# Optimization experiments

Hardware: AMD Instinct MI355X
Metric: run time of the kernel (lower is better)

Reference implementation:

```python
import jax, jax.numpy as jnp
import numpy as np

B, C, H, W = 4, 32, 544, 960


def setup_inputs() -> dict:
    key = jax.random.key(0)
    k1, k2, k3 = jax.random.split(key, 3)
    tenInput = jax.random.normal(k1, (B, C, H, W), dtype=jnp.float32)
    # flows of a few pixels magnitude, typical for adjacent video frames
    tenFlow = jax.random.normal(k2, (B, 2, H, W), dtype=jnp.float32) * 4.0
    tenMetric = jax.random.normal(k3, (B, 1, H, W), dtype=jnp.float32)
    return {"tenInput": tenInput, "tenFlow": tenFlow, "tenMetric": tenMetric}


def _splat_one(x, flow):
    # x: [C', H, W] values to splat; flow: [2, H, W] (dx, dy)
    Cp, h, w = x.shape
    gy, gx = jnp.meshgrid(jnp.arange(h, dtype=flow.dtype),
                          jnp.arange(w, dtype=flow.dtype), indexing='ij')
    ox = gx + flow[0]  # fractional target x
    oy = gy + flow[1]  # fractional target y
    x0 = jnp.floor(ox)
    y0 = jnp.floor(oy)
    x1 = x0 + 1.0
    y1 = y0 + 1.0
    # bilinear corner weights (NW, NE, SW, SE), identical to CUDA kernel
    w_nw = (x1 - ox) * (y1 - oy)
    w_ne = (ox - x0) * (y1 - oy)
    w_sw = (x1 - ox) * (oy - y0)
    w_se = (ox - x0) * (oy - y0)
    xf = x.reshape(Cp, h * w)
    out = jnp.zeros((Cp, h * w), dtype=x.dtype)
    for cx, cy, wt in ((x0, y0, w_nw), (x1, y0, w_ne), (x0, y1, w_sw), (x1, y1, w_se)):
        ix = cx.astype(jnp.int32)
        iy = cy.astype(jnp.int32)
        valid = (ix >= 0) & (ix < w) & (iy >= 0) & (iy < h)
        wt = jnp.where(valid, wt, 0.0).reshape(h * w)
        idx = (jnp.clip(iy, 0, h - 1) * w + jnp.clip(ix, 0, w - 1)).reshape(h * w)
        out = out.at[:, idx].add(xf * wt[None, :])
    return out.reshape(Cp, h, w)


def softsplat(tenInput, tenFlow, tenMetric, strType):
    if strType == 'average':
        x = jnp.concatenate([tenInput, jnp.ones_like(tenInput[:, :1])], axis=1)
    elif strType == 'linear':
        x = jnp.concatenate([tenInput * tenMetric, tenMetric], axis=1)
    elif strType == 'softmax':
        m = jnp.exp(tenMetric)
        x = jnp.concatenate([tenInput * m, m], axis=1)
    else:  # 'summation'
        x = tenInput
    out = jax.vmap(_splat_one)(x, tenFlow)
    if strType != 'summation':
        norm = out[:, -1:]
        norm = jnp.where(norm == 0.0, 1.0, norm)  # tenNormalize[tenNormalize==0]=1
        out = out[:, :-1] / norm
    return out


def reference(tenInput, tenFlow, tenMetric):
    return softsplat(tenInput, tenFlow, tenMetric, 'softmax')
```

## Files before the change

### kernel.cpp

```cpp
#include <hip/hip_runtime.h>
#include <hip/hip_fp16.h>

constexpr int B = 4, C = 32, H = 544, W = 960;
constexpr int HW = H * W;
constexpr int NPIX = B * HW;

constexpr int TX = 64, TY = 32;
constexpr int PAD = 16;
constexpr int WSX = TX + 2 * PAD;
constexpr int WSY = TY + 2 * PAD;
constexpr int WPIX = WSX * WSY;
constexpr int TILES_X = W / TX;
constexpr int TILES_Y = H / TY;
constexpr int NTILES = TILES_X * TILES_Y;
constexpr int TILE = TX * TY;
constexpr int TPB = 1024;
constexpr int NW = TPB / 64;
constexpr int PPT = TILE / TPB;
constexpr int WIT = WPIX / TPB;
constexpr int CAPE = 11264;
constexpr int MAXFAR = 64;
constexpr unsigned FARCAP = 32768;

struct FarEntry { unsigned key; float a; int p; };

__global__ __launch_bounds__(256)
void far_scan(const float* __restrict__ flow,
              const float* __restrict__ metric,
              unsigned* __restrict__ counter,
              FarEntry* __restrict__ fl)
{
    int idx = blockIdx.x * blockDim.x + threadIdx.x;
    if (idx >= NPIX) return;
    int b = idx / HW;
    int p = idx - b * HW;
    int y = p / W;
    int x = p - y * W;

    float fx = flow[(size_t)(b * 2 + 0) * HW + p];
    float fy = flow[(size_t)(b * 2 + 1) * HW + p];
    if (fabsf(fx) <= 14.0f && fabsf(fy) <= 14.0f) return;

    float ox = (float)x + fx, oy = (float)y + fy;
    float x0f = floorf(ox), y0f = floorf(oy);
    int x0 = (int)x0f, y0 = (int)y0f;
    float wxh = ox - x0f, wxl = 1.0f - wxh;
    float wyh = oy - y0f, wyl = 1.0f - wyh;
    const int   cxs[4] = { x0, x0 + 1, x0,     x0 + 1 };
    const int   cys[4] = { y0, y0,     y0 + 1, y0 + 1 };
    const float wts[4] = { wxl * wyl, wxh * wyl, wxl * wyh, wxh * wyh };
    float m = __expf(metric[(size_t)b * HW + p]);

#pragma unroll
    for (int k = 0; k < 4; ++k) {
        int cx = cxs[k], cy = cys[k];
        if ((unsigned)cx >= (unsigned)W || (unsigned)cy >= (unsigned)H) continue;
        int tx0 = (cx >> 6) << 6;
        int ty0 = (cy >> 5) << 5;
        bool catchable = (x >= tx0 - PAD) && (x < tx0 + TX + PAD) &&
                         (y >= ty0 - PAD) && (y < ty0 + TY + PAD);
        if (!catchable) {
            unsigned slot = atomicAdd(counter, 1u);
            if (slot < FARCAP) {
                int tile = (cy >> 5) * TILES_X + (cx >> 6);
                unsigned lidx = (unsigned)(((cy - ty0) << 6) | (cx - tx0));
                fl[slot] = { ((unsigned)(b * NTILES + tile) << 11) | lidx,
                             wts[k] * m, p };
            }
        }
    }
}

__global__ __launch_bounds__(TPB)
void splat_csr(const float* __restrict__ inp,
               const float* __restrict__ flow,
               const float* __restrict__ metric,
               const unsigned* __restrict__ counter,
               const FarEntry* __restrict__ fl,
               float* __restrict__ out)
{
    __shared__ unsigned entries[CAPE];
    __shared__ unsigned pool[WPIX + MAXFAR];
    __shared__ int farPix[MAXFAR];
    __shared__ unsigned wsum[NW];
    __shared__ unsigned farCnt;

    unsigned* offs = pool;
    __half2*  win  = reinterpret_cast<__half2*>(pool);

    const int t    = threadIdx.x;
    const int tile = blockIdx.x;
    const int b    = blockIdx.y;
    const int tx0  = (tile % TILES_X) * TX;
    const int ty0  = (tile / TILES_X) * TY;
    const unsigned btid = (unsigned)(b * NTILES + tile);

    const float* fxp = flow + (size_t)(b * 2 + 0) * HW;
    const float* fyp = flow + (size_t)(b * 2 + 1) * HW;
    const float* mp  = metric + (size_t)b * HW;

    for (int i = t; i < TILE; i += TPB) offs[i] = 0;
    if (t == 0) farCnt = 0;
    __syncthreads();

#pragma unroll
    for (int j = 0; j < WIT; ++j) {
        int i = t + j * TPB;
        int wx = i % WSX, wy = i / WSX;
        int gx = tx0 - PAD + wx, gy = ty0 - PAD + wy;
        if ((unsigned)gx >= (unsigned)W || (unsigned)gy >= (unsigned)H) continue;
        int p = gy * W + gx;
        float ox = (float)gx + fxp[p];
        float oy = (float)gy + fyp[p];
        int lx0 = (int)floorf(ox) - tx0, ly0 = (int)floorf(oy) - ty0;
        if (lx0 < -1 || lx0 >= TX || ly0 < -1 || ly0 >= TY) continue;
#pragma unroll
        for (int k = 0; k < 4; ++k) {
            int lx = lx0 + (k & 1), ly = ly0 + (k >> 1);
            if ((unsigned)lx < (unsigned)TX && (unsigned)ly < (unsigned)TY)
                atomicAdd(&offs[(ly << 6) + lx], 1u);
        }
    }
    unsigned farN = *counter;
    if (farN > FARCAP) farN = FARCAP;
    for (unsigned e = t; e < farN; e += TPB) {
        unsigned k = fl[e].key;
        if ((k >> 11) == btid) atomicAdd(&offs[k & 2047u], 1u);
    }
    __syncthreads();

    {
        unsigned c0 = offs[2 * t], c1 = offs[2 * t + 1];
        unsigned s = c0 + c1;
        unsigned lane = t & 63, wv = t >> 6;
        unsigned incl = s;
#pragma unroll
        for (int d = 1; d < 64; d <<= 1) {
            unsigned u = __shfl_up(incl, d);
            if (lane >= (unsigned)d) incl += u;
        }
        if (lane == 63) wsum[wv] = incl;
        __syncthreads();
        if (t < 64) {
            unsigned v = (lane < NW) ? wsum[lane] : 0u;
            unsigned inc2 = v;
#pragma unroll
            for (int d = 1; d < 16; d <<= 1) {
                unsigned u = __shfl_up(inc2, d);
                if (lane >= (unsigned)d) inc2 += u;
            }
            if (lane < NW) wsum[lane] = inc2 - v;
        }
        __syncthreads();
        unsigned base = wsum[wv] + (incl - s);
        offs[2 * t]     = base;
        offs[2 * t + 1] = base + c0;
    }
    __syncthreads();

#pragma unroll
    for (int j = 0; j < WIT; ++j) {
        int i = t + j * TPB;
        int wx = i % WSX, wy = i / WSX;
        int gx = tx0 - PAD + wx, gy = ty0 - PAD + wy;
        if ((unsigned)gx >= (unsigned)W || (unsigned)gy >= (unsigned)H) continue;
        int p = gy * W + gx;
        float ox = (float)gx + fxp[p];
        float oy = (float)gy + fyp[p];
        float x0f = floorf(ox), y0f = floorf(oy);
        int lx0 = (int)x0f - tx0, ly0 = (int)y0f - ty0;
        if (lx0 < -1 || lx0 >= TX || ly0 < -1 || ly0 >= TY) continue;
        float wxh = ox - x0f, wxl = 1.0f - wxh;
        float wyh = oy - y0f, wyl = 1.0f - wyh;
        float m = __expf(mp[p]);
        const float w4[4] = { wxl * wyl, wxh * wyl, wxl * wyh, wxh * wyh };
#pragma unroll
        for (int k = 0; k < 4; ++k) {
            int lx = lx0 + (k & 1), ly = ly0 + (k >> 1);
            if ((unsigned)lx < (unsigned)TX && (unsigned)ly < (unsigned)TY) {
                unsigned pos = atomicAdd(&offs[(ly << 6) + lx], 1u);
                if (pos < CAPE) {
                    unsigned short ha = __half_as_ushort(__float2half(w4[k] * m));
                    entries[pos] = ((unsigned)i << 16) | (unsigned)ha;
                }
            }
        }
    }
    for (unsigned e = t; e < farN; e += TPB) {
        unsigned k = fl[e].key;
        if ((k >> 11) == btid) {
            unsigned pos = atomicAdd(&offs[k & 2047u], 1u);
            if (pos < CAPE) {
                unsigned idx = atomicAdd(&farCnt, 1u);
                if (idx < MAXFAR) {
                    farPix[idx] = fl[e].p;
                    unsigned short ha = __half_as_ushort(__float2half(fl[e].a));
                    entries[pos] = ((unsigned)(WPIX + idx) << 16) | (unsigned)ha;
                } else {
                    entries[pos] = 0u;
                }
            }
        }
    }
    __syncthreads();

    int qout[PPT];
    unsigned es[PPT], ee[PPT];
    float rn[PPT];
#pragma unroll
    for (int k = 0; k < PPT; ++k) {
        int sp = t + k * TPB;
        qout[k] = (ty0 + (sp >> 6)) * W + tx0 + (sp & 63);
        unsigned end = min(offs[sp], (unsigned)CAPE);
        unsigned start = min(sp ? offs[sp - 1] : 0u, (unsigned)CAPE);
        if (start > end) start = end;
        es[k] = start; ee[k] = end;
        float n = 0.0f;
        for (unsigned e = start; e < end; ++e)
            n += __half2float(__ushort_as_half((unsigned short)(entries[e] & 0xFFFFu)));
        rn[k] = (n == 0.0f) ? 1.0f : 1.0f / n;
    }

    int wp[WIT];
#pragma unroll
    for (int j = 0; j < WIT; ++j) {
        int i = t + j * TPB;
        int wx = i % WSX, wy = i / WSX;
        int gx = tx0 - PAD + wx, gy = ty0 - PAD + wy;
        wp[j] = ((unsigned)gx < (unsigned)W && (unsigned)gy < (unsigned)H)
                ? gy * W + gx : -1;
    }

    float2 pre[WIT];
    {
        const float* t0 = inp + (size_t)(b * C) * HW;
        const float* t1 = t0 + HW;
#pragma unroll
        for (int j = 0; j < WIT; ++j)
            pre[j] = (wp[j] >= 0) ? make_float2(t0[wp[j]], t1[wp[j]])
                                  : make_float2(0.f, 0.f);
    }
    unsigned nFar = farCnt;
    if (nFar > MAXFAR) nFar = MAXFAR;
    __syncthreads();

    for (int cp = 0; cp < C / 2; ++cp) {
        const float* s0 = inp + (size_t)(b * C + 2 * cp) * HW;
        const float* s1 = s0 + HW;

#pragma unroll
        for (int j = 0; j < WIT; ++j)
            win[t + j * TPB] = __floats2half2_rn(pre[j].x, pre[j].y);
        if (t < nFar) {
            int p = farPix[t];
            win[WPIX + t] = __floats2half2_rn(s0[p], s1[p]);
        }
        __syncthreads();

        if (cp + 1 < C / 2) {
            const float* t0 = inp + (size_t)(b * C + 2 * (cp + 1)) * HW;
            const float* t1 = t0 + HW;
#pragma unroll
            for (int j = 0; j < WIT; ++j)
                pre[j] = (wp[j] >= 0) ? make_float2(t0[wp[j]], t1[wp[j]])
                                      : make_float2(0.f, 0.f);
        }

        float* o0 = out + (size_t)(b * C + 2 * cp) * HW;
        float* o1 = o0 + HW;
#pragma unroll
        for (int k = 0; k < PPT; ++k) {
            __half2 acc = __floats2half2_rn(0.f, 0.f);
            for (unsigned e = es[k]; e < ee[k]; ++e) {
                unsigned ent = entries[e];
                __half2 hv = win[ent >> 16];
                __half  w  = __ushort_as_half((unsigned short)(ent & 0xFFFFu));
                acc = __hfma2(__half2half2(w), hv, acc);
            }
            int q = qout[k];
            o0[q] = __low2float(acc)  * rn[k];
            o1[q] = __high2float(acc) * rn[k];
        }
        __syncthreads();
    }
}


__global__ __launch_bounds__(256)
void splat_f32(const float* __restrict__ inp,
               const float* __restrict__ flow,
               const float* __restrict__ metric,
               float* __restrict__ out,
               float* __restrict__ norm)
{
    int idx = blockIdx.x * blockDim.x + threadIdx.x;
    if (idx >= NPIX) return;
    int b = idx / HW;
    int p = idx - b * HW;
    int y = p / W;
    int x = p - y * W;

    float fx = flow[(b * 2 + 0) * HW + p];
    float fy = flow[(b * 2 + 1) * HW + p];
    float m  = __expf(metric[b * HW + p]);

    float ox = (float)x + fx, oy = (float)y + fy;
    float x0f = floorf(ox), y0f = floorf(oy);
    int x0 = (int)x0f, y0 = (int)y0f;
    float wx1 = ox - x0f, wx0 = 1.0f - wx1;
    float wy1 = oy - y0f, wy0 = 1.0f - wy1;

    float vm[C];
    const float* inb = inp + (size_t)b * C * HW + p;
#pragma unroll
    for (int c = 0; c < C; ++c) vm[c] = inb[(size_t)c * HW] * m;

    float* outb = out + (size_t)b * C * HW;
    float* nrmb = norm + (size_t)b * HW;

    const int   cxs[4] = { x0, x0 + 1, x0,     x0 + 1 };
    const int   cys[4] = { y0, y0,     y0 + 1, y0 + 1 };
    const float wts[4] = { wx0 * wy0, wx1 * wy0, wx0 * wy1, wx1 * wy1 };

#pragma unroll
    for (int k = 0; k < 4; ++k) {
        int cx = cxs[k], cy = cys[k];
        if (cx < 0 || cx >= W || cy < 0 || cy >= H) continue;
        float wt = wts[k];
        int q = cy * W + cx;
        atomicAdd(&nrmb[q], m * wt);
#pragma unroll
        for (int c = 0; c < C; ++c)
            atomicAdd(&outb[(size_t)c * HW + q], vm[c] * wt);
    }
}

__global__ __launch_bounds__(256)
void normalize_f32(float* __restrict__ out, const float* __restrict__ norm)
{
    int t = blockIdx.x * blockDim.x + threadIdx.x;
    long long base = (long long)t * 4;
    if (base >= (long long)B * C * HW) return;
    long long b = base / ((long long)C * HW);
    long long q = base % HW;

    float4 o = *reinterpret_cast<float4*>(out + base);
    float4 n = *reinterpret_cast<const float4*>(norm + b * HW + q);
    o.x /= (n.x == 0.0f ? 1.0f : n.x);
    o.y /= (n.y == 0.0f ? 1.0f : n.y);
    o.z /= (n.z == 0.0f ? 1.0f : n.z);
    o.w /= (n.w == 0.0f ? 1.0f : n.w);
    *reinterpret_cast<float4*>(out + base) = o;
}

extern "C" void kernel_launch(void* const* d_in, const int* in_sizes, int n_in,
                              void* d_out, int out_size, void* d_ws, size_t ws_size,
                              hipStream_t stream) {
    const float* tenInput  = (const float*)d_in[0];
    const float* tenFlow   = (const float*)d_in[1];
    const float* tenMetric = (const float*)d_in[2];
    float* out = (float*)d_out;

    const size_t need = 16 + (size_t)FARCAP * sizeof(FarEntry);

    if (ws_size >= need) {
        unsigned* counter = (unsigned*)d_ws;
        FarEntry* fl = (FarEntry*)((char*)d_ws + 16);

        hipMemsetAsync(counter, 0, 16, stream);
        far_scan<<<(NPIX + 255) / 256, 256, 0, stream>>>(tenFlow, tenMetric, counter, fl);

        dim3 grid(NTILES, B);
        splat_csr<<<grid, TPB, 0, stream>>>(tenInput, tenFlow, tenMetric,
                                            counter, fl, out);
    } else {
        float* norm = (float*)d_ws;
        hipMemsetAsync(out, 0, (size_t)B * C * HW * sizeof(float), stream);
        hipMemsetAsync(norm, 0, (size_t)NPIX * sizeof(float), stream);

        int threads = 256;
        int blocks = (NPIX + threads - 1) / threads;
        splat_f32<<<blocks, threads, 0, stream>>>(tenInput, tenFlow, tenMetric, out, norm);

        long long total = (long long)B * C * HW / 4;
        normalize_f32<<<(int)((total + threads - 1) / threads), threads, 0, stream>>>(out, norm);
    }
}
```

Baseline: 205.4 us.

## Process four channels per pass and shrink halo padding to cut passes

The gather loop now handles four fp16 channels per pass instead of two, packing them into a uint2 shared-memory window. This halves the number of passes, barriers and CSR entry walks per tile. The halo pad drops from 16 to 12, which shrinks the window and the entry capacity so shared memory fits the doubled window. The far-scan threshold follows the new pad, so more pixels take the slower far-list path, and WIT becomes a ceiling division with bounds checks.

```diff
diff --git a/kernel.cpp b/kernel.cpp
--- a/kernel.cpp
+++ b/kernel.cpp
@@ -6,7 +6,7 @@
 constexpr int NPIX = B * HW;
 
 constexpr int TX = 64, TY = 32;
-constexpr int PAD = 16;
+constexpr int PAD = 12;
 constexpr int WSX = TX + 2 * PAD;
 constexpr int WSY = TY + 2 * PAD;
 constexpr int WPIX = WSX * WSY;
@@ -17,9 +17,11 @@
 constexpr int TPB = 1024;
 constexpr int NW = TPB / 64;
 constexpr int PPT = TILE / TPB;
-constexpr int WIT = WPIX / TPB;
-constexpr int CAPE = 11264;
+constexpr int WIT = (WPIX + TPB - 1) / TPB;
+constexpr int CAPE = 9728;
 constexpr int MAXFAR = 64;
+constexpr int NCH = 4;
+constexpr int NPASS = C / NCH;
 constexpr unsigned FARCAP = 32768;
 
 struct FarEntry { unsigned key; float a; int p; };
@@ -39,7 +41,7 @@
 
     float fx = flow[(size_t)(b * 2 + 0) * HW + p];
     float fy = flow[(size_t)(b * 2 + 1) * HW + p];
-    if (fabsf(fx) <= 14.0f && fabsf(fy) <= 14.0f) return;
+    if (fabsf(fx) <= (float)(PAD - 2) && fabsf(fy) <= (float)(PAD - 2)) return;
 
     float ox = (float)x + fx, oy = (float)y + fy;
     float x0f = floorf(ox), y0f = floorf(oy);
@@ -80,13 +82,13 @@
                float* __restrict__ out)
 {
     __shared__ unsigned entries[CAPE];
-    __shared__ unsigned pool[WPIX + MAXFAR];
+    __shared__ __align__(16) unsigned pool[2 * (WPIX + MAXFAR)];
     __shared__ int farPix[MAXFAR];
     __shared__ unsigned wsum[NW];
     __shared__ unsigned farCnt;
 
     unsigned* offs = pool;
-    __half2*  win  = reinterpret_cast<__half2*>(pool);
+    uint2*    win2 = reinterpret_cast<uint2*>(pool);
 
     const int t    = threadIdx.x;
     const int tile = blockIdx.x;
@@ -106,6 +108,7 @@
 #pragma unroll
     for (int j = 0; j < WIT; ++j) {
         int i = t + j * TPB;
+        if (i >= WPIX) break;
         int wx = i % WSX, wy = i / WSX;
         int gx = tx0 - PAD + wx, gy = ty0 - PAD + wy;
         if ((unsigned)gx >= (unsigned)W || (unsigned)gy >= (unsigned)H) continue;
@@ -161,6 +164,7 @@
 #pragma unroll
     for (int j = 0; j < WIT; ++j) {
         int i = t + j * TPB;
+        if (i >= WPIX) break;
         int wx = i % WSX, wy = i / WSX;
         int gx = tx0 - PAD + wx, gy = ty0 - PAD + wy;
         if ((unsigned)gx >= (unsigned)W || (unsigned)gy >= (unsigned)H) continue;
@@ -225,61 +229,78 @@
 #pragma unroll
     for (int j = 0; j < WIT; ++j) {
         int i = t + j * TPB;
-        int wx = i % WSX, wy = i / WSX;
-        int gx = tx0 - PAD + wx, gy = ty0 - PAD + wy;
-        wp[j] = ((unsigned)gx < (unsigned)W && (unsigned)gy < (unsigned)H)
-                ? gy * W + gx : -1;
-    }
-
-    float2 pre[WIT];
+        wp[j] = -1;
+        if (i < WPIX) {
+            int wx = i % WSX, wy = i / WSX;
+            int gx = tx0 - PAD + wx, gy = ty0 - PAD + wy;
+            if ((unsigned)gx < (unsigned)W && (unsigned)gy < (unsigned)H)
+                wp[j] = gy * W + gx;
+        }
+    }
+
+    float4 pre[WIT];
     {
-        const float* t0 = inp + (size_t)(b * C) * HW;
-        const float* t1 = t0 + HW;
+        const float* s0 = inp + (size_t)(b * C) * HW;
 #pragma unroll
         for (int j = 0; j < WIT; ++j)
-            pre[j] = (wp[j] >= 0) ? make_float2(t0[wp[j]], t1[wp[j]])
-                                  : make_float2(0.f, 0.f);
+            pre[j] = (wp[j] >= 0)
+                   ? make_float4(s0[wp[j]], s0[HW + wp[j]],
+                                 s0[2 * HW + wp[j]], s0[3 * HW + wp[j]])
+                   : make_float4(0.f, 0.f, 0.f, 0.f);
     }
     unsigned nFar = farCnt;
     if (nFar > MAXFAR) nFar = MAXFAR;
     __syncthreads();
 
-    for (int cp = 0; cp < C / 2; ++cp) {
-        const float* s0 = inp + (size_t)(b * C + 2 * cp) * HW;
-        const float* s1 = s0 + HW;
-
-#pragma unroll
-        for (int j = 0; j < WIT; ++j)
-            win[t + j * TPB] = __floats2half2_rn(pre[j].x, pre[j].y);
+    for (int cp = 0; cp < NPASS; ++cp) {
+        const float* s0 = inp + (size_t)(b * C + NCH * cp) * HW;
+
+#pragma unroll
+        for (int j = 0; j < WIT; ++j) {
+            int i = t + j * TPB;
+            if (i < WPIX) {
+                __half2 h01 = __floats2half2_rn(pre[j].x, pre[j].y);
+                __half2 h23 = __floats2half2_rn(pre[j].z, pre[j].w);
+                win2[i] = make_uint2(*reinterpret_cast<unsigned*>(&h01),
+                                     *reinterpret_cast<unsigned*>(&h23));
+            }
+        }
         if (t < nFar) {
             int p = farPix[t];
-            win[WPIX + t] = __floats2half2_rn(s0[p], s1[p]);
+            __half2 h01 = __floats2half2_rn(s0[p], s0[HW + p]);
+            __half2 h23 = __floats2half2_rn(s0[2 * HW + p], s0[3 * HW + p]);
+            win2[WPIX + t] = make_uint2(*reinterpret_cast<unsigned*>(&h01),
+                                        *reinterpret_cast<unsigned*>(&h23));
         }
         __syncthreads();
 
-        if (cp + 1 < C / 2) {
-            const float* t0 = inp + (size_t)(b * C + 2 * (cp + 1)) * HW;
-            const float* t1 = t0 + HW;
+        if (cp + 1 < NPASS) {
+            const float* n0 = inp + (size_t)(b * C + NCH * (cp + 1)) * HW;
 #pragma unroll
             for (int j = 0; j < WIT; ++j)
-                pre[j] = (wp[j] >= 0) ? make_float2(t0[wp[j]], t1[wp[j]])
-                                      : make_float2(0.f, 0.f);
-        }
-
-        float* o0 = out + (size_t)(b * C + 2 * cp) * HW;
-        float* o1 = o0 + HW;
+                pre[j] = (wp[j] >= 0)
+                       ? make_float4(n0[wp[j]], n0[HW + wp[j]],
+                                     n0[2 * HW + wp[j]], n0[3 * HW + wp[j]])
+                       : make_float4(0.f, 0.f, 0.f, 0.f);
+        }
+
+        float* o0 = out + (size_t)(b * C + NCH * cp) * HW;
 #pragma unroll
         for (int k = 0; k < PPT; ++k) {
-            __half2 acc = __floats2half2_rn(0.f, 0.f);
+            __half2 a01 = __floats2half2_rn(0.f, 0.f);
+            __half2 a23 = __floats2half2_rn(0.f, 0.f);
             for (unsigned e = es[k]; e < ee[k]; ++e) {
                 unsigned ent = entries[e];
-                __half2 hv = win[ent >> 16];
-                __half  w  = __ushort_as_half((unsigned short)(ent & 0xFFFFu));
-                acc = __hfma2(__half2half2(w), hv, acc);
+                uint2 wv = win2[ent >> 16];
+                __half2 w2 = __half2half2(__ushort_as_half((unsigned short)(ent & 0xFFFFu)));
+                a01 = __hfma2(w2, *reinterpret_cast<__half2*>(&wv.x), a01);
+                a23 = __hfma2(w2, *reinterpret_cast<__half2*>(&wv.y), a23);
             }
             int q = qout[k];
-            o0[q] = __low2float(acc)  * rn[k];
-            o1[q] = __high2float(acc) * rn[k];
+            o0[q]          = __low2float(a01)  * rn[k];
+            o0[HW + q]     = __high2float(a01) * rn[k];
+            o0[2 * HW + q] = __low2float(a23)  * rn[k];
+            o0[3 * HW + q] = __high2float(a23) * rn[k];
         }
         __syncthreads();
     }
```

Result: faster. 198.4 us (-3.4%).

## Gather source values directly from global memory instead of staging half2 windows in LDS

Applied to the files above, without the earlier changes.

Drops the per-channel-pair shared-memory window of half2 source values and its barriers. Each output pixel now walks its CSR entry list and gathers fp32 inputs straight from global memory for 8 channels at a time, accumulating in fp32. Corner weights are now cached in registers during the counting pass so the fill pass does not recompute flow, and the padding shrinks from 16 to 12, which reduces both the window and the entry capacity. The trade is that LDS reuse of the window is replaced by repeated global or cache gathers. It also relies on the far-scan path to catch the larger set of long-range flows that the smaller padding no longer covers.

```diff
diff --git a/kernel.cpp b/kernel.cpp
--- a/kernel.cpp
+++ b/kernel.cpp
@@ -6,7 +6,7 @@
 constexpr int NPIX = B * HW;
 
 constexpr int TX = 64, TY = 32;
-constexpr int PAD = 16;
+constexpr int PAD = 12;
 constexpr int WSX = TX + 2 * PAD;
 constexpr int WSY = TY + 2 * PAD;
 constexpr int WPIX = WSX * WSY;
@@ -17,9 +17,11 @@
 constexpr int TPB = 1024;
 constexpr int NW = TPB / 64;
 constexpr int PPT = TILE / TPB;
-constexpr int WIT = WPIX / TPB;
-constexpr int CAPE = 11264;
+constexpr int WIT = (WPIX + TPB - 1) / TPB;
+constexpr int CAPE = 9728;
 constexpr int MAXFAR = 64;
+constexpr int NCH = 8;
+constexpr int NPASS = C / NCH;
 constexpr unsigned FARCAP = 32768;
 
 struct FarEntry { unsigned key; float a; int p; };
@@ -39,7 +41,7 @@
 
     float fx = flow[(size_t)(b * 2 + 0) * HW + p];
     float fy = flow[(size_t)(b * 2 + 1) * HW + p];
-    if (fabsf(fx) <= 14.0f && fabsf(fy) <= 14.0f) return;
+    if (fabsf(fx) <= (float)(PAD - 2) && fabsf(fy) <= (float)(PAD - 2)) return;
 
     float ox = (float)x + fx, oy = (float)y + fy;
     float x0f = floorf(ox), y0f = floorf(oy);
@@ -80,19 +82,17 @@
                float* __restrict__ out)
 {
     __shared__ unsigned entries[CAPE];
-    __shared__ unsigned pool[WPIX + MAXFAR];
+    __shared__ unsigned offs[TILE];
     __shared__ int farPix[MAXFAR];
     __shared__ unsigned wsum[NW];
     __shared__ unsigned farCnt;
-
-    unsigned* offs = pool;
-    __half2*  win  = reinterpret_cast<__half2*>(pool);
 
     const int t    = threadIdx.x;
     const int tile = blockIdx.x;
     const int b    = blockIdx.y;
     const int tx0  = (tile % TILES_X) * TX;
     const int ty0  = (tile / TILES_X) * TY;
+    const int rowBase = (ty0 - PAD) * W + (tx0 - PAD);
     const unsigned btid = (unsigned)(b * NTILES + tile);
 
     const float* fxp = flow + (size_t)(b * 2 + 0) * HW;
@@ -103,64 +103,13 @@
     if (t == 0) farCnt = 0;
     __syncthreads();
 
+    unsigned cr[WIT][4];
 #pragma unroll
     for (int j = 0; j < WIT; ++j) {
+#pragma unroll
+        for (int k = 0; k < 4; ++k) cr[j][k] = 0xFFFF0000u;
         int i = t + j * TPB;
-        int wx = i % WSX, wy = i / WSX;
-        int gx = tx0 - PAD + wx, gy = ty0 - PAD + wy;
-        if ((unsigned)gx >= (unsigned)W || (unsigned)gy >= (unsigned)H) continue;
-        int p = gy * W + gx;
-        float ox = (float)gx + fxp[p];
-        float oy = (float)gy + fyp[p];
-        int lx0 = (int)floorf(ox) - tx0, ly0 = (int)floorf(oy) - ty0;
-        if (lx0 < -1 || lx0 >= TX || ly0 < -1 || ly0 >= TY) continue;
-#pragma unroll
-        for (int k = 0; k < 4; ++k) {
-            int lx = lx0 + (k & 1), ly = ly0 + (k >> 1);
-            if ((unsigned)lx < (unsigned)TX && (unsigned)ly < (unsigned)TY)
-                atomicAdd(&offs[(ly << 6) + lx], 1u);
-        }
-    }
-    unsigned farN = *counter;
-    if (farN > FARCAP) farN = FARCAP;
-    for (unsigned e = t; e < farN; e += TPB) {
-        unsigned k = fl[e].key;
-        if ((k >> 11) == btid) atomicAdd(&offs[k & 2047u], 1u);
-    }
-    __syncthreads();
-
-    {
-        unsigned c0 = offs[2 * t], c1 = offs[2 * t + 1];
-        unsigned s = c0 + c1;
-        unsigned lane = t & 63, wv = t >> 6;
-        unsigned incl = s;
-#pragma unroll
-        for (int d = 1; d < 64; d <<= 1) {
-            unsigned u = __shfl_up(incl, d);
-            if (lane >= (unsigned)d) incl += u;
-        }
-        if (lane == 63) wsum[wv] = incl;
-        __syncthreads();
-        if (t < 64) {
-            unsigned v = (lane < NW) ? wsum[lane] : 0u;
-            unsigned inc2 = v;
-#pragma unroll
-            for (int d = 1; d < 16; d <<= 1) {
-                unsigned u = __shfl_up(inc2, d);
-                if (lane >= (unsigned)d) inc2 += u;
-            }
-            if (lane < NW) wsum[lane] = inc2 - v;
-        }
-        __syncthreads();
-        unsigned base = wsum[wv] + (incl - s);
-        offs[2 * t]     = base;
-        offs[2 * t + 1] = base + c0;
-    }
-    __syncthreads();
-
-#pragma unroll
-    for (int j = 0; j < WIT; ++j) {
-        int i = t + j * TPB;
+        if (i >= WPIX) continue;
         int wx = i % WSX, wy = i / WSX;
         int gx = tx0 - PAD + wx, gy = ty0 - PAD + wy;
         if ((unsigned)gx >= (unsigned)W || (unsigned)gy >= (unsigned)H) continue;
@@ -178,11 +127,63 @@
         for (int k = 0; k < 4; ++k) {
             int lx = lx0 + (k & 1), ly = ly0 + (k >> 1);
             if ((unsigned)lx < (unsigned)TX && (unsigned)ly < (unsigned)TY) {
-                unsigned pos = atomicAdd(&offs[(ly << 6) + lx], 1u);
-                if (pos < CAPE) {
-                    unsigned short ha = __half_as_ushort(__float2half(w4[k] * m));
-                    entries[pos] = ((unsigned)i << 16) | (unsigned)ha;
-                }
+                unsigned lidx = (unsigned)((ly << 6) + lx);
+                unsigned short ha = __half_as_ushort(__float2half(w4[k] * m));
+                cr[j][k] = (lidx << 16) | (unsigned)ha;
+                atomicAdd(&offs[lidx], 1u);
+            }
+        }
+    }
+    unsigned farN = *counter;
+    if (farN > FARCAP) farN = FARCAP;
+    for (unsigned e = t; e < farN; e += TPB) {
+        unsigned k = fl[e].key;
+        if ((k >> 11) == btid) atomicAdd(&offs[k & 2047u], 1u);
+    }
+    __syncthreads();
+
+    {
+        unsigned c0 = offs[2 * t], c1 = offs[2 * t + 1];
+        unsigned s = c0 + c1;
+        unsigned lane = t & 63, wv = t >> 6;
+        unsigned incl = s;
+#pragma unroll
+        for (int d = 1; d < 64; d <<= 1) {
+            unsigned u = __shfl_up(incl, d);
+            if (lane >= (unsigned)d) incl += u;
+        }
+        if (lane == 63) wsum[wv] = incl;
+        __syncthreads();
+        if (t < 64) {
+            unsigned v = (lane < NW) ? wsum[lane] : 0u;
+            unsigned inc2 = v;
+#pragma unroll
+            for (int d = 1; d < 16; d <<= 1) {
+                unsigned u = __shfl_up(inc2, d);
+                if (lane >= (unsigned)d) inc2 += u;
+            }
+            if (lane < NW) wsum[lane] = inc2 - v;
+        }
+        __syncthreads();
+        unsigned base = wsum[wv] + (incl - s);
+        offs[2 * t]     = base;
+        offs[2 * t + 1] = base + c0;
+    }
+    __syncthreads();
+
+#pragma unroll
+    for (int j = 0; j < WIT; ++j) {
+        int i = t + j * TPB;
+        unsigned wx = (unsigned)(i % WSX), wy = (unsigned)(i / WSX);
+        unsigned top = (wy << 7) | wx;
+#pragma unroll
+        for (int k = 0; k < 4; ++k) {
+            unsigned c = cr[j][k];
+            unsigned lidx = c >> 16;
+            if (lidx != 0xFFFFu) {
+                unsigned pos = atomicAdd(&offs[lidx], 1u);
+                if (pos < CAPE)
+                    entries[pos] = (top << 16) | (c & 0xFFFFu);
             }
         }
     }
@@ -195,9 +196,9 @@
                 if (idx < MAXFAR) {
                     farPix[idx] = fl[e].p;
                     unsigned short ha = __half_as_ushort(__float2half(fl[e].a));
-                    entries[pos] = ((unsigned)(WPIX + idx) << 16) | (unsigned)ha;
+                    entries[pos] = ((0x8000u | idx) << 16) | (unsigned)ha;
                 } else {
-                    entries[pos] = 0u;
+                    entries[pos] = (((unsigned)PAD << 7 | (unsigned)PAD) << 16);
                 }
             }
         }
@@ -220,68 +221,32 @@
             n += __half2float(__ushort_as_half((unsigned short)(entries[e] & 0xFFFFu)));
         rn[k] = (n == 0.0f) ? 1.0f : 1.0f / n;
     }
-
-    int wp[WIT];
-#pragma unroll
-    for (int j = 0; j < WIT; ++j) {
-        int i = t + j * TPB;
-        int wx = i % WSX, wy = i / WSX;
-        int gx = tx0 - PAD + wx, gy = ty0 - PAD + wy;
-        wp[j] = ((unsigned)gx < (unsigned)W && (unsigned)gy < (unsigned)H)
-                ? gy * W + gx : -1;
-    }
-
-    float2 pre[WIT];
-    {
-        const float* t0 = inp + (size_t)(b * C) * HW;
-        const float* t1 = t0 + HW;
-#pragma unroll
-        for (int j = 0; j < WIT; ++j)
-            pre[j] = (wp[j] >= 0) ? make_float2(t0[wp[j]], t1[wp[j]])
-                                  : make_float2(0.f, 0.f);
-    }
-    unsigned nFar = farCnt;
-    if (nFar > MAXFAR) nFar = MAXFAR;
-    __syncthreads();
-
-    for (int cp = 0; cp < C / 2; ++cp) {
-        const float* s0 = inp + (size_t)(b * C + 2 * cp) * HW;
-        const float* s1 = s0 + HW;
-
-#pragma unroll
-        for (int j = 0; j < WIT; ++j)
-            win[t + j * TPB] = __floats2half2_rn(pre[j].x, pre[j].y);
-        if (t < nFar) {
-            int p = farPix[t];
-            win[WPIX + t] = __floats2half2_rn(s0[p], s1[p]);
-        }
-        __syncthreads();
-
-        if (cp + 1 < C / 2) {
-            const float* t0 = inp + (size_t)(b * C + 2 * (cp + 1)) * HW;
-            const float* t1 = t0 + HW;
-#pragma unroll
-            for (int j = 0; j < WIT; ++j)
-                pre[j] = (wp[j] >= 0) ? make_float2(t0[wp[j]], t1[wp[j]])
-                                      : make_float2(0.f, 0.f);
-        }
-
-        float* o0 = out + (size_t)(b * C + 2 * cp) * HW;
-        float* o1 = o0 + HW;
+    __syncthreads();
+
+    for (int cp = 0; cp < NPASS; ++cp) {
+        const float* s = inp + (size_t)(b * C + NCH * cp) * HW;
+        float* o = out + (size_t)(b * C + NCH * cp) * HW;
 #pragma unroll
         for (int k = 0; k < PPT; ++k) {
-            __half2 acc = __floats2half2_rn(0.f, 0.f);
+            float a[NCH];
+#pragma unroll
+            for (int c = 0; c < NCH; ++c) a[c] = 0.f;
             for (unsigned e = es[k]; e < ee[k]; ++e) {
                 unsigned ent = entries[e];
-                __half2 hv = win[ent >> 16];
-                __half  w  = __ushort_as_half((unsigned short)(ent & 0xFFFFu));
-                acc = __hfma2(__half2half2(w), hv, acc);
+                unsigned top = ent >> 16;
+                float w = __half2float(__ushort_as_half((unsigned short)(ent & 0xFFFFu)));
+                int p;
+                if (top & 0x8000u) p = farPix[top & 63u];
+                else               p = rowBase + (int)(top >> 7) * W + (int)(top & 127u);
+#pragma unroll
+                for (int c = 0; c < NCH; ++c)
+                    a[c] = fmaf(w, s[(size_t)c * HW + p], a[c]);
             }
             int q = qout[k];
-            o0[q] = __low2float(acc)  * rn[k];
-            o1[q] = __high2float(acc) * rn[k];
-        }
-        __syncthreads();
+#pragma unroll
+            for (int c = 0; c < NCH; ++c)
+                o[(size_t)c * HW + q] = a[c] * rn[k];
+        }
     }
 }
 
```

Result: slower. 784.8 us (+282.1%).
